# Kernel tuning notes

Measured on AMD Instinct MI355X. Metric: run time of the kernel, lower is better.

The kernel has to match this reference:

```python
import jax, jax.numpy as jnp
import numpy as np

B, S, D, DOUT, E = 2, 2048, 1024, 1024, 8
DH = 4 * D  # expert hidden size


def setup_inputs() -> dict:
    key = jax.random.key(0)
    ks = jax.random.split(key, 7)
    sc = lambda *sh: 1.0 / np.sqrt(sh[-2]) if len(sh) >= 2 else 0.02
    return {
        "x": jax.random.normal(ks[0], (B, S, D), jnp.float32),
        "Wg": jax.random.normal(ks[1], (D, E), jnp.float32) / np.sqrt(D),
        "bg": jnp.zeros((E,), jnp.float32),
        "W1": jax.random.normal(ks[2], (E, D, DH), jnp.float32) / np.sqrt(D),
        "b1": jax.random.normal(ks[3], (E, DH), jnp.float32) * 0.02,
        "W2": jax.random.normal(ks[4], (E, DH, DOUT), jnp.float32) / np.sqrt(DH),
        "b2": jax.random.normal(ks[5], (E, DOUT), jnp.float32) * 0.02,
    }


def reference(x, Wg, bg, W1, b1, W2, b2):
    # x: [B, S, D] -> flatten tokens (chunking over seq in the original is
    # math-neutral: routing and expert MLP are per-token).
    Bb, Ss, Dd = x.shape
    xt = x.reshape(-1, Dd)                       # [T, D]
    # Gate: softmax then argmax (top-1 routing, output NOT scaled by gate prob)
    gates = jax.nn.softmax(xt @ Wg + bg, axis=-1)  # [T, E]
    sel = jnp.argmax(gates, axis=-1)               # [T]
    nE = W1.shape[0]
    out = jnp.zeros((xt.shape[0], W2.shape[-1]), x.dtype)
    # Grouped expert MLP expressed as masked dense loop over the small fixed
    # expert count (jit-friendly; a fused gather-grouped-GEMM-scatter kernel
    # is the optimization target).
    for e in range(nE):
        h = jax.nn.gelu(xt @ W1[e] + b1[e], approximate=False)  # [T, 4D]
        ye = h @ W2[e] + b2[e]                                  # [T, DOUT]
        out = jnp.where((sel == e)[:, None], ye, out)
    return out.reshape(Bb, Ss, -1)
```

## Files before the change

### kernel.cpp

```cpp
#include <hip/hip_runtime.h>
#include <hip/hip_bf16.h>
#include <math.h>

#define T_TOK 4096
#define DIM   1024
#define NEXP  8
#define DHID  4096
#define NDOUT 1024
#define BM2   256
#define MAXT  24

typedef short bf16x8 __attribute__((ext_vector_type(8)));
typedef float f32x4 __attribute__((ext_vector_type(4)));

__device__ __forceinline__ unsigned short f2bf(float f) {
  unsigned u = __float_as_uint(f);
  u += 0x7fffu + ((u >> 16) & 1u);
  return (unsigned short)(u >> 16);
}
__device__ __forceinline__ unsigned pack2bf(float a, float b) {
  return (unsigned)f2bf(a) | ((unsigned)f2bf(b) << 16);
}
__device__ __forceinline__ void gl_lds16(const void* g, void* l) {
  __builtin_amdgcn_global_load_lds(
      (const __attribute__((address_space(1))) void*)g,
      (__attribute__((address_space(3))) void*)l, 16, 0, 0);
}
__device__ __forceinline__ float gelu_fast(float h) {
  float z  = 0.79788456080286536f * (h + 0.044715f * h * h * h);
  float az = fabsf(z);
  float et = __expf(-2.0f * az);
  float th = (1.0f - et) / (1.0f + et);
  th = copysignf(th, z);
  return 0.5f * h * (1.0f + th);
}

__global__ __launch_bounds__(256)
void gate_kernel(const float* __restrict__ x, const float* __restrict__ Wg,
                 const float* __restrict__ bg, int* __restrict__ sel,
                 unsigned short* __restrict__ xbf) {
  int lane = threadIdx.x & 63;
  int wid  = threadIdx.x >> 6;
  int t = blockIdx.x * 4 + wid;
  if (t >= T_TOK) return;
  const float* xr = x + (size_t)t * DIM;
  unsigned short* xbr = xbf + (size_t)t * DIM;
  double acc[NEXP];
#pragma unroll
  for (int e = 0; e < NEXP; e++) acc[e] = 0.0;
#pragma unroll
  for (int j = 0; j < 4; j++) {
    int d0 = j * 256 + lane * 4;
    float4 v = *(const float4*)(xr + d0);
    uint2 p; p.x = pack2bf(v.x, v.y); p.y = pack2bf(v.z, v.w);
    *(uint2*)(xbr + d0) = p;
    float xs[4] = {v.x, v.y, v.z, v.w};
#pragma unroll
    for (int i = 0; i < 4; i++) {
      const float4* wr = reinterpret_cast<const float4*>(Wg + (size_t)(d0 + i) * NEXP);
      float4 w0 = wr[0], w1 = wr[1];
      double xv = (double)xs[i];
      acc[0] += xv * (double)w0.x;
      acc[1] += xv * (double)w0.y;
      acc[2] += xv * (double)w0.z;
      acc[3] += xv * (double)w0.w;
      acc[4] += xv * (double)w1.x;
      acc[5] += xv * (double)w1.y;
      acc[6] += xv * (double)w1.z;
      acc[7] += xv * (double)w1.w;
    }
  }
#pragma unroll
  for (int off = 32; off >= 1; off >>= 1) {
#pragma unroll
    for (int e = 0; e < NEXP; e++) acc[e] += __shfl_down(acc[e], off);
  }
  if (lane == 0) {
    double best = acc[0] + (double)bg[0];
    int bi = 0;
#pragma unroll
    for (int e = 1; e < NEXP; e++) {
      double v = acc[e] + (double)bg[e];
      if (v > best) { best = v; bi = e; }
    }
    sel[t] = bi;
  }
}

__global__ void zero_kernel(int* __restrict__ counts) {
  if (threadIdx.x < NEXP) counts[threadIdx.x] = 0;
}

__global__ void hist_kernel(const int* __restrict__ sel, int* __restrict__ counts) {
  __shared__ int lc[NEXP];
  if (threadIdx.x < NEXP) lc[threadIdx.x] = 0;
  __syncthreads();
  int t = blockIdx.x * 256 + threadIdx.x;
  atomicAdd(&lc[sel[t]], 1);
  __syncthreads();
  if (threadIdx.x < NEXP) atomicAdd(&counts[threadIdx.x], lc[threadIdx.x]);
}

__global__ void plan_kernel(const int* __restrict__ counts, int* __restrict__ base,
                            int* __restrict__ cursor, int* __restrict__ tileExpert,
                            int* __restrict__ tilePos, int* __restrict__ tileRows,
                            int* __restrict__ ntiles) {
  if (threadIdx.x == 0) {
    int acc = 0, nt = 0;
    for (int e = 0; e < NEXP; e++) {
      base[e] = acc; cursor[e] = acc;
      int c = counts[e];
      for (int j = 0; j < c; j += BM2) {
        tileExpert[nt] = e;
        tilePos[nt]    = acc + j;
        int rem = c - j;
        tileRows[nt]   = rem < BM2 ? rem : BM2;
        nt++;
      }
      acc += c;
    }
    *ntiles = nt;
  }
}

__global__ void scatter_kernel(const int* __restrict__ sel, int* __restrict__ cursor,
                               int* __restrict__ list) {
  __shared__ int lcnt[NEXP];
  __shared__ int lbase[NEXP];
  int tid = threadIdx.x;
  if (tid < NEXP) lcnt[tid] = 0;
  __syncthreads();
  int t = blockIdx.x * 256 + tid;
  int e = sel[t];
  int lpos = atomicAdd(&lcnt[e], 1);
  __syncthreads();
  if (tid < NEXP) lbase[tid] = atomicAdd(&cursor[tid], lcnt[tid]);
  __syncthreads();
  list[lbase[e] + lpos] = t;
}

__global__ __launch_bounds__(256)
void transpose_tile_kernel(const float* __restrict__ in, unsigned short* __restrict__ out,
                           int K, int N) {
  int nb = blockIdx.x, kb = blockIdx.y, e = blockIdx.z;
  const float* inp = in + (size_t)e * K * N;
  __shared__ unsigned short lds[128][72];
  int tx = threadIdx.x;
  int kloc = tx >> 5;
  int n4   = (tx & 31) << 2;
#pragma unroll
  for (int p = 0; p < 8; p++) {
    int k = p * 8 + kloc;
    float4 v = *(const float4*)(inp + (size_t)(kb * 64 + k) * N + nb * 128 + n4);
    lds[n4 + 0][k] = f2bf(v.x);
    lds[n4 + 1][k] = f2bf(v.y);
    lds[n4 + 2][k] = f2bf(v.z);
    lds[n4 + 3][k] = f2bf(v.w);
  }
  __syncthreads();
  char* tile = (char*)(out + (((size_t)e * gridDim.x + nb) * gridDim.y + kb) * 8192);
  int r  = tx >> 1;
  int kc0 = (tx & 1) * 32;
#pragma unroll
  for (int c = 0; c < 4; c++) {
    int kc = kc0 + c * 8;
    uint4 v = *(const uint4*)&lds[r][kc];
    *(uint4*)(tile + r * 128 + ((2 * kc) ^ ((r & 7) << 4))) = v;
  }
}


__global__ __launch_bounds__(1024)
void gemm1_kernel(const unsigned short* __restrict__ xbf, const unsigned short* __restrict__ W1T,
                  const float* __restrict__ b1, const int* __restrict__ list,
                  const int* __restrict__ tileExpert, const int* __restrict__ tilePos,
                  const int* __restrict__ tileRows, const int* __restrict__ ntiles,
                  unsigned short* __restrict__ HcT) {
  int tIdx = blockIdx.y;
  if (tIdx >= *ntiles) return;
  int e = tileExpert[tIdx], posBase = tilePos[tIdx], rows = tileRows[tIdx];
  int nb = blockIdx.x;

  __shared__ __align__(1024) char SH[65536];
  char* As = SH;
  char* Bs = SH + 32768;

  const int tx = threadIdx.x, lane = tx & 63, w = tx >> 6;
  const int wm = w >> 2, wn = w & 3;

  const int arow = tx >> 3;
  const int px = (((tx & 7) ^ (arow & 7)) << 4);
  const char* aSrc[2];
#pragma unroll
  for (int j = 0; j < 2; j++) {
    int r = arow + j * 128;
    int tok = list[posBase + (r < rows ? r : rows - 1)];
    aSrc[j] = (const char*)xbf + (size_t)tok * (DIM * 2) + px;
  }
  const char* b0 = (const char*)W1T + ((size_t)(e * 32 + nb * 2) * 16) * 16384 + tx * 16;
  const char* b1p = b0 + 16 * 16384;

  f32x4 acc[4][4];
#pragma unroll
  for (int mf = 0; mf < 4; mf++)
#pragma unroll
    for (int nf = 0; nf < 4; nf++)
      acc[mf][nf] = f32x4{0.f, 0.f, 0.f, 0.f};

  const int NT = DIM / 64;
  for (int kt = 0; kt < NT; kt++) {
    gl_lds16(aSrc[0] + kt * 128, As + tx * 16);
    gl_lds16(aSrc[1] + kt * 128, As + 16384 + tx * 16);
    gl_lds16(b0 + kt * 16384, Bs + tx * 16);
    gl_lds16(b1p + kt * 16384, Bs + 16384 + tx * 16);
    __syncthreads();
#pragma unroll
    for (int ks = 0; ks < 2; ks++) {
      int koff = ks * 64 + ((lane >> 4) << 4);
      bf16x8 aF[4], bF[4];
#pragma unroll
      for (int mf = 0; mf < 4; mf++) {
        int row = wm * 64 + mf * 16 + (lane & 15);
        aF[mf] = *(const bf16x8*)(As + row * 128 + (koff ^ ((row & 7) << 4)));
      }
#pragma unroll
      for (int nf = 0; nf < 4; nf++) {
        int n = wn * 64 + nf * 16 + (lane & 15);
        bF[nf] = *(const bf16x8*)(Bs + n * 128 + (koff ^ ((n & 7) << 4)));
      }
#pragma unroll
      for (int mf = 0; mf < 4; mf++)
#pragma unroll
        for (int nf = 0; nf < 4; nf++)
          acc[mf][nf] = __builtin_amdgcn_mfma_f32_16x16x32_bf16(aF[mf], bF[nf], acc[mf][nf], 0, 0, 0);
    }
    __syncthreads();
  }

  const float* b1e = b1 + (size_t)e * DHID;
#pragma unroll
  for (int p = 0; p < 2; p++) {
    if ((wn >> 1) == p) {
      char* region = SH + ((wn & 1) << 15);
#pragma unroll
      for (int nf = 0; nf < 4; nf++) {
        int kloc = nf * 16 + (lane & 15);
        float bias = b1e[nb * 256 + wn * 64 + kloc];
#pragma unroll
        for (int mf = 0; mf < 4; mf++) {
#pragma unroll
          for (int j = 0; j < 4; j++) {
            int row = wm * 64 + mf * 16 + ((lane >> 4) << 2) + j;
            float g = gelu_fast(acc[mf][nf][j] + bias);
            *(unsigned short*)(region + row * 128 + ((2 * kloc) ^ ((row & 7) << 4))) = f2bf(g);
          }
        }
      }
    }
    __syncthreads();
    int img = tx >> 9;
    int off = (tx & 511) * 64;
    const char* src = SH + img * 32768 + off;
    char* dst = (char*)HcT + (((size_t)tIdx * 64) + nb * 4 + p * 2 + img) * 32768 + off;
#pragma unroll
    for (int i = 0; i < 4; i++)
      *(uint4*)(dst + i * 16) = *(const uint4*)(src + i * 16);
    __syncthreads();
  }
}

__global__ __launch_bounds__(1024)
void gemm2_kernel(const unsigned short* __restrict__ HcT, const unsigned short* __restrict__ W2T,
                  const float* __restrict__ b2, const int* __restrict__ tileExpert,
                  const int* __restrict__ tilePos, const int* __restrict__ tileRows,
                  const int* __restrict__ ntiles, float* __restrict__ Ppart) {
  int tIdx = blockIdx.y;
  if (tIdx >= *ntiles) return;
  int e = tileExpert[tIdx], posBase = tilePos[tIdx], rows = tileRows[tIdx];
  int nb = blockIdx.x;
  int zs = blockIdx.z;

  __shared__ __align__(1024) char SH[65536];
  char* As = SH;
  char* Bs = SH + 32768;

  const int tx = threadIdx.x, lane = tx & 63, w = tx >> 6;
  const int wm = w >> 2, wn = w & 3;

  const char* aT = (const char*)HcT + ((size_t)tIdx * 64 + zs * 16) * 32768 + tx * 16;
  const char* b0 = (const char*)W2T + ((size_t)(e * 8 + nb * 2) * 64 + zs * 16) * 16384 + tx * 16;
  const char* b1p = b0 + 64 * 16384;

  f32x4 acc[4][4];
#pragma unroll
  for (int mf = 0; mf < 4; mf++)
#pragma unroll
    for (int nf = 0; nf < 4; nf++)
      acc[mf][nf] = f32x4{0.f, 0.f, 0.f, 0.f};

  const int NT = 16;
  for (int kt = 0; kt < NT; kt++) {
    gl_lds16(aT + kt * 32768, As + tx * 16);
    gl_lds16(aT + kt * 32768 + 16384, As + 16384 + tx * 16);
    gl_lds16(b0 + kt * 16384, Bs + tx * 16);
    gl_lds16(b1p + kt * 16384, Bs + 16384 + tx * 16);
    __syncthreads();
#pragma unroll
    for (int ks = 0; ks < 2; ks++) {
      int koff = ks * 64 + ((lane >> 4) << 4);
      bf16x8 aF[4], bF[4];
#pragma unroll
      for (int mf = 0; mf < 4; mf++) {
        int row = wm * 64 + mf * 16 + (lane & 15);
        aF[mf] = *(const bf16x8*)(As + row * 128 + (koff ^ ((row & 7) << 4)));
      }
#pragma unroll
      for (int nf = 0; nf < 4; nf++) {
        int n = wn * 64 + nf * 16 + (lane & 15);
        bF[nf] = *(const bf16x8*)(Bs + n * 128 + (koff ^ ((n & 7) << 4)));
      }
#pragma unroll
      for (int mf = 0; mf < 4; mf++)
#pragma unroll
        for (int nf = 0; nf < 4; nf++)
          acc[mf][nf] = __builtin_amdgcn_mfma_f32_16x16x32_bf16(aF[mf], bF[nf], acc[mf][nf], 0, 0, 0);
    }
    __syncthreads();
  }

  const float* b2e = b2 + (size_t)e * NDOUT;
  float* P = Ppart + (size_t)zs * T_TOK * NDOUT;
#pragma unroll
  for (int nf = 0; nf < 4; nf++) {
    int col = nb * 256 + wn * 64 + nf * 16 + (lane & 15);
    float bias = (zs == 0) ? b2e[col] : 0.f;
#pragma unroll
    for (int mf = 0; mf < 4; mf++)
#pragma unroll
      for (int j = 0; j < 4; j++) {
        int rloc = wm * 64 + mf * 16 + ((lane >> 4) << 2) + j;
        if (rloc < rows)
          P[(size_t)(posBase + rloc) * NDOUT + col] = acc[mf][nf][j] + bias;
      }
  }
}

__global__ __launch_bounds__(256)
void reduce_kernel(const float* __restrict__ Ppart, const int* __restrict__ list,
                   float* __restrict__ out) {
  int pos = blockIdx.x;
  int tok = list[pos];
  int c = threadIdx.x * 4;
  float4 s = *(const float4*)(Ppart + (size_t)pos * NDOUT + c);
#pragma unroll
  for (int z = 1; z < 4; z++) {
    float4 a = *(const float4*)(Ppart + (size_t)z * T_TOK * NDOUT + (size_t)pos * NDOUT + c);
    s.x += a.x; s.y += a.y; s.z += a.z; s.w += a.w;
  }
  *(float4*)(out + (size_t)tok * NDOUT + c) = s;
}

extern "C" void kernel_launch(void* const* d_in, const int* in_sizes, int n_in,
                              void* d_out, int out_size, void* d_ws, size_t ws_size,
                              hipStream_t stream) {
  const float* x  = (const float*)d_in[0];
  const float* Wg = (const float*)d_in[1];
  const float* bg = (const float*)d_in[2];
  const float* W1 = (const float*)d_in[3];
  const float* b1 = (const float*)d_in[4];
  const float* W2 = (const float*)d_in[5];
  const float* b2 = (const float*)d_in[6];
  float* out = (float*)d_out;

  char* ws = (char*)d_ws;
  int* sel        = (int*)(ws);
  int* counts     = (int*)(ws + 16384);
  int* base       = (int*)(ws + 16448);
  int* cursor     = (int*)(ws + 16512);
  int* ntiles     = (int*)(ws + 16576);
  int* tileExpert = (int*)(ws + 16640);
  int* tilePos    = (int*)(ws + 16832);
  int* tileRows   = (int*)(ws + 17024);
  int* list       = (int*)(ws + 17408);

  unsigned short* xbf = (unsigned short*)(ws + (1ull << 20));
  unsigned short* HcT = (unsigned short*)(ws + (10ull << 20));
  unsigned short* W1T = (unsigned short*)(ws + (58ull << 20));
  unsigned short* W2T = (unsigned short*)(ws + (122ull << 20));
  float* Ppart        = (float*)(ws + (58ull << 20));

  gate_kernel<<<T_TOK / 4, 256, 0, stream>>>(x, Wg, bg, sel, xbf);
  zero_kernel<<<1, 64, 0, stream>>>(counts);
  hist_kernel<<<T_TOK / 256, 256, 0, stream>>>(sel, counts);
  plan_kernel<<<1, 64, 0, stream>>>(counts, base, cursor, tileExpert, tilePos, tileRows, ntiles);
  scatter_kernel<<<T_TOK / 256, 256, 0, stream>>>(sel, cursor, list);

  transpose_tile_kernel<<<dim3(DHID / 128, DIM / 64, NEXP), 256, 0, stream>>>(W1, W1T, DIM, DHID);
  transpose_tile_kernel<<<dim3(NDOUT / 128, DHID / 64, NEXP), 256, 0, stream>>>(W2, W2T, DHID, NDOUT);

  gemm1_kernel<<<dim3(DHID / 256, MAXT), 1024, 0, stream>>>(
      xbf, W1T, b1, list, tileExpert, tilePos, tileRows, ntiles, HcT);
  gemm2_kernel<<<dim3(NDOUT / 256, MAXT, 4), 1024, 0, stream>>>(
      HcT, W2T, b2, tileExpert, tilePos, tileRows, ntiles, Ppart);
  reduce_kernel<<<T_TOK, 256, 0, stream>>>(Ppart, list, out);
}
```

Measured before the change: 348.0 us.

## Double-buffer LDS tiles in grouped GEMMs to overlap global loads with MFMA

Both grouped GEMM kernels now use two 64KB LDS stages (128KB total). The next K-tile is issued via global_load_lds before the current tile is computed, with explicit vmcnt waits and raw s_barrier/sched_barrier in place of __syncthreads. This is meant to hide global memory latency behind MFMA work, at the cost of doubling LDS usage to 128KB per block, which fits within MI355X's 160KB LDS. It also relies on hand-counted vmcnt values and s_barrier placement being correct.

New measurement: 317.3 us. 8.8% less time.

```diff
diff --git a/kernel.cpp b/kernel.cpp
--- a/kernel.cpp
+++ b/kernel.cpp
@@ -26,6 +26,8 @@
       (const __attribute__((address_space(1))) void*)g,
       (__attribute__((address_space(3))) void*)l, 16, 0, 0);
 }
+#define SBAR()  __builtin_amdgcn_s_barrier()
+#define SCHED() __builtin_amdgcn_sched_barrier(0)
 __device__ __forceinline__ float gelu_fast(float h) {
   float z  = 0.79788456080286536f * (h + 0.044715f * h * h * h);
   float az = fabsf(z);
@@ -170,7 +172,7 @@
 }
 
 
-__global__ __launch_bounds__(1024)
+__global__ __launch_bounds__(1024, 1)
 void gemm1_kernel(const unsigned short* __restrict__ xbf, const unsigned short* __restrict__ W1T,
                   const float* __restrict__ b1, const int* __restrict__ list,
                   const int* __restrict__ tileExpert, const int* __restrict__ tilePos,
@@ -181,9 +183,7 @@
   int e = tileExpert[tIdx], posBase = tilePos[tIdx], rows = tileRows[tIdx];
   int nb = blockIdx.x;
 
-  __shared__ __align__(1024) char SH[65536];
-  char* As = SH;
-  char* Bs = SH + 32768;
+  __shared__ __align__(1024) char SH[131072];
 
   const int tx = threadIdx.x, lane = tx & 63, w = tx >> 6;
   const int wm = w >> 2, wn = w & 3;
@@ -200,20 +200,25 @@
   const char* b0 = (const char*)W1T + ((size_t)(e * 32 + nb * 2) * 16) * 16384 + tx * 16;
   const char* b1p = b0 + 16 * 16384;
 
-  f32x4 acc[4][4];
-#pragma unroll
-  for (int mf = 0; mf < 4; mf++)
-#pragma unroll
-    for (int nf = 0; nf < 4; nf++)
-      acc[mf][nf] = f32x4{0.f, 0.f, 0.f, 0.f};
-
-  const int NT = DIM / 64;
-  for (int kt = 0; kt < NT; kt++) {
+  auto STAGE = [&](int buf, int kt) {
+    char* As = SH + buf * 65536;
+    char* Bs = As + 32768;
     gl_lds16(aSrc[0] + kt * 128, As + tx * 16);
     gl_lds16(aSrc[1] + kt * 128, As + 16384 + tx * 16);
     gl_lds16(b0 + kt * 16384, Bs + tx * 16);
     gl_lds16(b1p + kt * 16384, Bs + 16384 + tx * 16);
-    __syncthreads();
+  };
+
+  f32x4 acc[4][4];
+#pragma unroll
+  for (int mf = 0; mf < 4; mf++)
+#pragma unroll
+    for (int nf = 0; nf < 4; nf++)
+      acc[mf][nf] = f32x4{0.f, 0.f, 0.f, 0.f};
+
+  auto COMPUTE = [&](int buf) {
+    const char* As = SH + buf * 65536;
+    const char* Bs = As + 32768;
 #pragma unroll
     for (int ks = 0; ks < 2; ks++) {
       int koff = ks * 64 + ((lane >> 4) << 4);
@@ -234,7 +239,21 @@
         for (int nf = 0; nf < 4; nf++)
           acc[mf][nf] = __builtin_amdgcn_mfma_f32_16x16x32_bf16(aF[mf], bF[nf], acc[mf][nf], 0, 0, 0);
     }
-    __syncthreads();
+  };
+
+  const int NT = DIM / 64;
+  STAGE(0, 0);
+  for (int kt = 0; kt < NT; kt++) {
+    int buf = kt & 1;
+    if (kt + 1 < NT) {
+      STAGE(buf ^ 1, kt + 1);
+      asm volatile("s_waitcnt vmcnt(4)" ::: "memory");
+    } else {
+      asm volatile("s_waitcnt vmcnt(0)" ::: "memory");
+    }
+    SCHED(); SBAR(); SCHED();
+    COMPUTE(buf);
+    SCHED(); SBAR(); SCHED();
   }
 
   const float* b1e = b1 + (size_t)e * DHID;
@@ -269,7 +288,7 @@
   }
 }
 
-__global__ __launch_bounds__(1024)
+__global__ __launch_bounds__(1024, 1)
 void gemm2_kernel(const unsigned short* __restrict__ HcT, const unsigned short* __restrict__ W2T,
                   const float* __restrict__ b2, const int* __restrict__ tileExpert,
                   const int* __restrict__ tilePos, const int* __restrict__ tileRows,
@@ -280,9 +299,7 @@
   int nb = blockIdx.x;
   int zs = blockIdx.z;
 
-  __shared__ __align__(1024) char SH[65536];
-  char* As = SH;
-  char* Bs = SH + 32768;
+  __shared__ __align__(1024) char SH[131072];
 
   const int tx = threadIdx.x, lane = tx & 63, w = tx >> 6;
   const int wm = w >> 2, wn = w & 3;
@@ -291,20 +308,25 @@
   const char* b0 = (const char*)W2T + ((size_t)(e * 8 + nb * 2) * 64 + zs * 16) * 16384 + tx * 16;
   const char* b1p = b0 + 64 * 16384;
 
-  f32x4 acc[4][4];
-#pragma unroll
-  for (int mf = 0; mf < 4; mf++)
-#pragma unroll
-    for (int nf = 0; nf < 4; nf++)
-      acc[mf][nf] = f32x4{0.f, 0.f, 0.f, 0.f};
-
-  const int NT = 16;
-  for (int kt = 0; kt < NT; kt++) {
+  auto STAGE = [&](int buf, int kt) {
+    char* As = SH + buf * 65536;
+    char* Bs = As + 32768;
     gl_lds16(aT + kt * 32768, As + tx * 16);
     gl_lds16(aT + kt * 32768 + 16384, As + 16384 + tx * 16);
     gl_lds16(b0 + kt * 16384, Bs + tx * 16);
     gl_lds16(b1p + kt * 16384, Bs + 16384 + tx * 16);
-    __syncthreads();
+  };
+
+  f32x4 acc[4][4];
+#pragma unroll
+  for (int mf = 0; mf < 4; mf++)
+#pragma unroll
+    for (int nf = 0; nf < 4; nf++)
+      acc[mf][nf] = f32x4{0.f, 0.f, 0.f, 0.f};
+
+  auto COMPUTE = [&](int buf) {
+    const char* As = SH + buf * 65536;
+    const char* Bs = As + 32768;
 #pragma unroll
     for (int ks = 0; ks < 2; ks++) {
       int koff = ks * 64 + ((lane >> 4) << 4);
@@ -325,7 +347,21 @@
         for (int nf = 0; nf < 4; nf++)
           acc[mf][nf] = __builtin_amdgcn_mfma_f32_16x16x32_bf16(aF[mf], bF[nf], acc[mf][nf], 0, 0, 0);
     }
-    __syncthreads();
+  };
+
+  const int NT = 16;
+  STAGE(0, 0);
+  for (int kt = 0; kt < NT; kt++) {
+    int buf = kt & 1;
+    if (kt + 1 < NT) {
+      STAGE(buf ^ 1, kt + 1);
+      asm volatile("s_waitcnt vmcnt(4)" ::: "memory");
+    } else {
+      asm volatile("s_waitcnt vmcnt(0)" ::: "memory");
+    }
+    SCHED(); SBAR(); SCHED();
+    COMPUTE(buf);
+    SCHED(); SBAR(); SCHED();
   }
 
   const float* b2e = b2 + (size_t)e * NDOUT;
```
